# Kernel optimization log

Hardware: AMD Instinct MI355X
Metric: run time of the kernel (lower is better)

The kernel has to match this reference:

```python
import jax, jax.numpy as jnp
import numpy as np

N = 50000
E = 800000
F_IN = 128
HID = 128
NCLS = 40


def setup_inputs() -> dict:
    key = jax.random.key(0)
    ks = jax.random.split(key, 12)
    def glorot(k, fan_in, fan_out):
        s = jnp.sqrt(6.0 / (fan_in + fan_out))
        return jax.random.uniform(k, (fan_in, fan_out), jnp.float32, -s, s)
    x = jax.random.normal(ks[0], (N, F_IN), jnp.float32)
    edge_index = jax.random.randint(ks[1], (2, E), 0, N, jnp.int64)
    W1 = glorot(ks[2], F_IN, HID); b1 = jnp.zeros((HID,), jnp.float32)
    W2 = glorot(ks[3], HID, HID);  b2 = jnp.zeros((HID,), jnp.float32)
    W3 = glorot(ks[4], HID, HID);  b3 = jnp.zeros((HID,), jnp.float32)
    Wc = glorot(ks[5], HID, NCLS)
    bc = jnp.zeros((NCLS,), jnp.float32)
    return {"x": x, "edge_index": edge_index, "W1": W1, "b1": b1,
            "W2": W2, "b2": b2, "W3": W3, "b3": b3, "Wc": Wc, "bc": bc}


def _gcn_conv(h, src, dst, norm, W, b):
    # GCNConv: linear transform, then normalized scatter-add aggregation
    h = h @ W                              # [N, out]
    msg = h[src] * norm[:, None]           # [E+N, out] gathered + scaled
    out = jax.ops.segment_sum(msg, dst, num_segments=N)
    return out + b


def reference(x, edge_index, W1, b1, W2, b2, W3, b3, Wc, bc):
    # add self-loops (PyG GCNConv default) and compute symmetric norm once
    loop = jnp.arange(N, dtype=edge_index.dtype)
    src = jnp.concatenate([edge_index[0], loop])
    dst = jnp.concatenate([edge_index[1], loop])
    deg = jax.ops.segment_sum(jnp.ones_like(dst, dtype=x.dtype), dst, num_segments=N)
    dinv = jax.lax.rsqrt(deg)              # deg >= 1 due to self-loops
    norm = dinv[src] * dinv[dst]           # [E+N]

    h = jax.nn.relu(_gcn_conv(x, src, dst, norm, W1, b1))
    h = jax.nn.relu(_gcn_conv(h, src, dst, norm, W2, b2))
    h = jax.nn.relu(_gcn_conv(h, src, dst, norm, W3, b3))
    out = h @ Wc + bc
    return (out, h)
```

## Files before the change

### kernel.cpp

```cpp
#include <hip/hip_runtime.h>
#include <hip/hip_fp16.h>


#define FEAT 128

typedef _Float16 half_t;
typedef _Float16 f16x8 __attribute__((ext_vector_type(8)));
typedef float f32x16 __attribute__((ext_vector_type(16)));


__global__ __launch_bounds__(256) void k_count_rank(const int* __restrict__ dst,
                                                    int* __restrict__ deg,
                                                    int* __restrict__ rank, int E) {
  int e = blockIdx.x * 256 + threadIdx.x;
  if (e < E) rank[e] = atomicAdd(&deg[dst[e]], 1);
}

__global__ __launch_bounds__(256) void k_scanA(const int* __restrict__ deg,
                                               int* __restrict__ partial, int N) {
  __shared__ int s[256];
  int t = threadIdx.x;
  int i = blockIdx.x * 256 + t;
  s[t] = (i < N) ? deg[i] : 0;
  __syncthreads();
  for (int off = 128; off > 0; off >>= 1) {
    if (t < off) s[t] += s[t + off];
    __syncthreads();
  }
  if (t == 0) partial[blockIdx.x] = s[0];
}

__global__ __launch_bounds__(256) void k_scanB(int* __restrict__ partial, int nblk,
                                               int* __restrict__ offsets, int N) {
  __shared__ int s[256];
  int t = threadIdx.x;
  int v = (t < nblk) ? partial[t] : 0;
  s[t] = v;
  __syncthreads();
  for (int off = 1; off < 256; off <<= 1) {
    int x = (t >= off) ? s[t - off] : 0;
    __syncthreads();
    s[t] += x;
    __syncthreads();
  }
  if (t < nblk) partial[t] = s[t] - v;
  if (t == 0) offsets[N] = s[255];
}

__global__ __launch_bounds__(256) void k_scanC(const int* __restrict__ deg,
                                               const int* __restrict__ partial,
                                               int* __restrict__ offsets,
                                               float* __restrict__ dinv, int N) {
  __shared__ int s[256];
  int t = threadIdx.x;
  int i = blockIdx.x * 256 + t;
  int v = (i < N) ? deg[i] : 0;
  s[t] = v;
  __syncthreads();
  for (int off = 1; off < 256; off <<= 1) {
    int x = (t >= off) ? s[t - off] : 0;
    __syncthreads();
    s[t] += x;
    __syncthreads();
  }
  if (i < N) {
    offsets[i] = partial[blockIdx.x] + s[t] - v;
    dinv[i] = rsqrtf((float)(v + 1));
  }
}

__global__ __launch_bounds__(256) void k_place(const int* __restrict__ src,
                                               const int* __restrict__ dst,
                                               const int* __restrict__ offsets,
                                               const int* __restrict__ rank,
                                               int* __restrict__ col, int E) {
  int e = blockIdx.x * 256 + threadIdx.x;
  if (e < E) col[offsets[dst[e]] + rank[e]] = src[e];
}


__global__ __launch_bounds__(256) void k_prepW(const float* __restrict__ W1,
                                               const float* __restrict__ W2,
                                               const float* __restrict__ W3,
                                               half_t* __restrict__ Wt1,
                                               half_t* __restrict__ Wt2,
                                               half_t* __restrict__ Wt3) {
  int idx = blockIdx.x * 256 + threadIdx.x;
  int which = idx >> 14;
  int i = idx & 16383;
  int k = i >> 7, n = i & 127;
  const float* W = (which == 0) ? W1 : (which == 1) ? W2 : W3;
  half_t* Wt = (which == 0) ? Wt1 : (which == 1) ? Wt2 : Wt3;
  Wt[n * 128 + k] = (half_t)W[i];
}

template <int SRC_FP32>
__global__ __launch_bounds__(128) void k_gemm_mfma(const void* __restrict__ Asrc,
                                                   const half_t* __restrict__ Wt,
                                                   const float* __restrict__ dinv,
                                                   half_t* __restrict__ T,
                                                   int nrows) {
  __shared__ char lds[65536];
  char* sA = lds;
  char* sW = lds + 32768;
  int t = threadIdx.x;
  int rowBase = blockIdx.x * 128;
  int rowsHere = min(128, nrows - rowBase);

  #pragma unroll
  for (int i = 0; i < 16; ++i) {
    int lin = t + i * 128;
    int r = lin >> 4, c = lin & 15;
    *(float4*)(sW + r * 256 + ((c * 16) ^ ((r & 15) << 4))) =
        *(const float4*)((const char*)Wt + r * 256 + c * 16);
  }
  if (SRC_FP32) {
    const float* Af = (const float*)Asrc;
    #pragma unroll
    for (int i = 0; i < 16; ++i) {
      int lin = t + i * 128;
      int r = lin >> 4, c = lin & 15;
      f16x8 h = {};
      if (r < rowsHere) {
        const float4* p = (const float4*)(Af + (size_t)(rowBase + r) * FEAT + c * 8);
        float4 v0 = p[0], v1 = p[1];
        h[0] = (half_t)v0.x; h[1] = (half_t)v0.y; h[2] = (half_t)v0.z; h[3] = (half_t)v0.w;
        h[4] = (half_t)v1.x; h[5] = (half_t)v1.y; h[6] = (half_t)v1.z; h[7] = (half_t)v1.w;
      }
      *(f16x8*)(sA + r * 256 + ((c * 16) ^ ((r & 15) << 4))) = h;
    }
  } else {
    const char* Ah = (const char*)Asrc;
    #pragma unroll
    for (int i = 0; i < 16; ++i) {
      int lin = t + i * 128;
      int r = lin >> 4, c = lin & 15;
      float4 v = {};
      if (r < rowsHere) v = *(const float4*)(Ah + (size_t)(rowBase + r) * 256 + c * 16);
      *(float4*)(sA + r * 256 + ((c * 16) ^ ((r & 15) << 4))) = v;
    }
  }
  __syncthreads();

  int wv = t >> 6;
  int l = t & 63;
  int l31 = l & 31;
  int lhi = l >> 5;
  int sw = (l31 & 15) << 4;

  f32x16 acc[2][4] = {};

  #pragma unroll
  for (int step = 0; step < 8; ++step) {
    int koff = step * 32 + lhi * 16;
    int ko = koff ^ sw;
    f16x8 a0 = *(const f16x8*)(sA + (wv * 64 + l31) * 256 + ko);
    f16x8 a1 = *(const f16x8*)(sA + (wv * 64 + 32 + l31) * 256 + ko);
    f16x8 b0 = *(const f16x8*)(sW + (l31) * 256 + ko);
    f16x8 b1 = *(const f16x8*)(sW + (32 + l31) * 256 + ko);
    f16x8 b2 = *(const f16x8*)(sW + (64 + l31) * 256 + ko);
    f16x8 b3 = *(const f16x8*)(sW + (96 + l31) * 256 + ko);
    acc[0][0] = __builtin_amdgcn_mfma_f32_32x32x16_f16(a0, b0, acc[0][0], 0, 0, 0);
    acc[0][1] = __builtin_amdgcn_mfma_f32_32x32x16_f16(a0, b1, acc[0][1], 0, 0, 0);
    acc[0][2] = __builtin_amdgcn_mfma_f32_32x32x16_f16(a0, b2, acc[0][2], 0, 0, 0);
    acc[0][3] = __builtin_amdgcn_mfma_f32_32x32x16_f16(a0, b3, acc[0][3], 0, 0, 0);
    acc[1][0] = __builtin_amdgcn_mfma_f32_32x32x16_f16(a1, b0, acc[1][0], 0, 0, 0);
    acc[1][1] = __builtin_amdgcn_mfma_f32_32x32x16_f16(a1, b1, acc[1][1], 0, 0, 0);
    acc[1][2] = __builtin_amdgcn_mfma_f32_32x32x16_f16(a1, b2, acc[1][2], 0, 0, 0);
    acc[1][3] = __builtin_amdgcn_mfma_f32_32x32x16_f16(a1, b3, acc[1][3], 0, 0, 0);
  }

  #pragma unroll
  for (int m = 0; m < 2; ++m) {
    #pragma unroll
    for (int j = 0; j < 16; ++j) {
      int rloc = wv * 64 + m * 32 + (j & 3) + 8 * (j >> 2) + 4 * lhi;
      if (rloc < rowsHere) {
        int grow = rowBase + rloc;
        float d = dinv[grow];
        #pragma unroll
        for (int n = 0; n < 4; ++n) {
          T[(size_t)grow * FEAT + n * 32 + l31] = (half_t)(acc[m][n][j] * d);
        }
      }
    }
  }
}

template <int OUTF>
__global__ __launch_bounds__(256) void k_aggregate(const __half2* __restrict__ T2,
                                                   const int* __restrict__ offsets,
                                                   const int* __restrict__ col,
                                                   const float* __restrict__ dinv,
                                                   const float* __restrict__ bias,
                                                   float* __restrict__ outF,
                                                   __half2* __restrict__ outH,
                                                   int N) {
  int wave = threadIdx.x >> 6;
  int lane = threadIdx.x & 63;
  int node = blockIdx.x * 4 + wave;
  if (node >= N) return;
  int e0 = offsets[node], e1 = offsets[node + 1];

  __half2 sv = T2[(size_t)node * 64 + lane];
  float ax = __half2float(sv.x), ay = __half2float(sv.y);

  int e = e0;
  for (; e + 8 <= e1; e += 8) {
    int s0 = col[e + 0], s1 = col[e + 1], s2 = col[e + 2], s3 = col[e + 3];
    int s4 = col[e + 4], s5 = col[e + 5], s6 = col[e + 6], s7 = col[e + 7];
    __half2 v0 = T2[(size_t)s0 * 64 + lane];
    __half2 v1 = T2[(size_t)s1 * 64 + lane];
    __half2 v2 = T2[(size_t)s2 * 64 + lane];
    __half2 v3 = T2[(size_t)s3 * 64 + lane];
    __half2 v4 = T2[(size_t)s4 * 64 + lane];
    __half2 v5 = T2[(size_t)s5 * 64 + lane];
    __half2 v6 = T2[(size_t)s6 * 64 + lane];
    __half2 v7 = T2[(size_t)s7 * 64 + lane];
    float x01 = __half2float(v0.x) + __half2float(v1.x);
    float x23 = __half2float(v2.x) + __half2float(v3.x);
    float x45 = __half2float(v4.x) + __half2float(v5.x);
    float x67 = __half2float(v6.x) + __half2float(v7.x);
    float y01 = __half2float(v0.y) + __half2float(v1.y);
    float y23 = __half2float(v2.y) + __half2float(v3.y);
    float y45 = __half2float(v4.y) + __half2float(v5.y);
    float y67 = __half2float(v6.y) + __half2float(v7.y);
    ax += (x01 + x23) + (x45 + x67);
    ay += (y01 + y23) + (y45 + y67);
  }
  for (; e + 2 <= e1; e += 2) {
    __half2 v0 = T2[(size_t)col[e] * 64 + lane];
    __half2 v1 = T2[(size_t)col[e + 1] * 64 + lane];
    ax += __half2float(v0.x) + __half2float(v1.x);
    ay += __half2float(v0.y) + __half2float(v1.y);
  }
  if (e < e1) {
    __half2 v = T2[(size_t)col[e] * 64 + lane];
    ax += __half2float(v.x);
    ay += __half2float(v.y);
  }

  float di = dinv[node];
  float2 b = ((const float2*)bias)[lane];
  float ox = fmaxf(di * ax + b.x, 0.f);
  float oy = fmaxf(di * ay + b.y, 0.f);
  if (OUTF) {
    *(float2*)&outF[(size_t)node * FEAT + 2 * lane] = make_float2(ox, oy);
  } else {
    outH[(size_t)node * 64 + lane] = __floats2half2_rn(ox, oy);
  }
}

__global__ __launch_bounds__(256) void k_classifier(const float* __restrict__ h,
                                                    const float* __restrict__ Wc,
                                                    const float* __restrict__ bc,
                                                    float* __restrict__ out, int N) {
  __shared__ float sh[64 * 132];
  __shared__ float sWt[40 * 130];
  int t = threadIdx.x;
  int nodeBase = blockIdx.x * 64;
  int nodesHere = min(64, N - nodeBase);

  for (int i = t; i < FEAT * 40; i += 256) {
    int k = i / 40, c = i - k * 40;
    sWt[c * 130 + k] = Wc[i];
  }
  {
    const float4* H4 = (const float4*)(h + (size_t)nodeBase * FEAT);
    #pragma unroll
    for (int i = 0; i < 8; ++i) {
      int lin = t + i * 256;
      int r = lin >> 5, kc = lin & 31;
      float4 v = make_float4(0.f, 0.f, 0.f, 0.f);
      if (r < nodesHere) v = H4[lin];
      *(float4*)&sh[r * 132 + kc * 4] = v;
    }
  }
  __syncthreads();

  int n0 = (t >> 3) * 2;
  int cg = (t & 7) * 5;
  float acc0[5], acc1[5];
  #pragma unroll
  for (int j = 0; j < 5; ++j) { acc0[j] = bc[cg + j]; acc1[j] = acc0[j]; }

  #pragma unroll 4
  for (int k4 = 0; k4 < 32; ++k4) {
    float4 h0 = *(const float4*)&sh[n0 * 132 + k4 * 4];
    float4 h1 = *(const float4*)&sh[(n0 + 1) * 132 + k4 * 4];
    #pragma unroll
    for (int j = 0; j < 5; ++j) {
      float4 w = *(const float4*)&sWt[(cg + j) * 130 + k4 * 4];
      acc0[j] += h0.x * w.x + h0.y * w.y + h0.z * w.z + h0.w * w.w;
      acc1[j] += h1.x * w.x + h1.y * w.y + h1.z * w.z + h1.w * w.w;
    }
  }

  if (n0 < nodesHere) {
    float* o = out + (size_t)(nodeBase + n0) * 40 + cg;
    #pragma unroll
    for (int j = 0; j < 5; ++j) o[j] = acc0[j];
  }
  if (n0 + 1 < nodesHere) {
    float* o = out + (size_t)(nodeBase + n0 + 1) * 40 + cg;
    #pragma unroll
    for (int j = 0; j < 5; ++j) o[j] = acc1[j];
  }
}


extern "C" void kernel_launch(void* const* d_in, const int* in_sizes, int n_in,
                              void* d_out, int out_size, void* d_ws, size_t ws_size,
                              hipStream_t stream) {
  const float* x    = (const float*)d_in[0];
  const int*   edge = (const int*)d_in[1];
  const float* W1   = (const float*)d_in[2];
  const float* b1   = (const float*)d_in[3];
  const float* W2   = (const float*)d_in[4];
  const float* b2   = (const float*)d_in[5];
  const float* W3   = (const float*)d_in[6];
  const float* b3   = (const float*)d_in[7];
  const float* Wc   = (const float*)d_in[8];
  const float* bc   = (const float*)d_in[9];

  int N = in_sizes[0] / FEAT;
  int E = in_sizes[1] / 2;

  float* out  = (float*)d_out;
  float* hOut = out + (size_t)N * 40;

  size_t o = 0;
  char* wsb = (char*)d_ws;
  auto take = [&](size_t bytes) -> void* {
    void* p = wsb + o;
    o += (bytes + 255) & ~(size_t)255;
    return p;
  };
  float*   dinv    = (float*)take((size_t)N * 4);
  int*     deg     = (int*)take((size_t)N * 4);
  int*     rank    = (int*)take((size_t)E * 4);
  int*     partial = (int*)take(256 * 4);
  int*     offsets = (int*)take(((size_t)N + 8) * 4);
  int*     col     = (int*)take((size_t)E * 4);
  half_t*  T2h     = (half_t*)take((size_t)N * FEAT * 2);
  half_t*  Bh      = (half_t*)take((size_t)N * FEAT * 2);
  half_t*  Wt1     = (half_t*)take(16384 * 2);
  half_t*  Wt2     = (half_t*)take(16384 * 2);
  half_t*  Wt3     = (half_t*)take(16384 * 2);

  const int* e_src = edge;
  const int* e_dst = edge + E;

  hipMemsetAsync(deg, 0, (size_t)N * 4, stream);

  int nblk = (N + 255) / 256;
  int eblk = (E + 255) / 256;

  k_prepW<<<192, 256, 0, stream>>>(W1, W2, W3, Wt1, Wt2, Wt3);
  k_count_rank<<<eblk, 256, 0, stream>>>(e_dst, deg, rank, E);
  k_scanA<<<nblk, 256, 0, stream>>>(deg, partial, N);
  k_scanB<<<1, 256, 0, stream>>>(partial, nblk, offsets, N);
  k_scanC<<<nblk, 256, 0, stream>>>(deg, partial, offsets, dinv, N);
  k_place<<<eblk, 256, 0, stream>>>(e_src, e_dst, offsets, rank, col, E);

  int gblk = (N + 127) / 128;
  int ablk = (N + 3) / 4;
  __half2* T2 = (__half2*)T2h;
  k_gemm_mfma<1><<<gblk, 128, 0, stream>>>(x, Wt1, dinv, T2h, N);
  k_aggregate<0><<<ablk, 256, 0, stream>>>(T2, offsets, col, dinv, b1, nullptr,
                                           (__half2*)Bh, N);
  k_gemm_mfma<0><<<gblk, 128, 0, stream>>>(Bh, Wt2, dinv, T2h, N);
  k_aggregate<0><<<ablk, 256, 0, stream>>>(T2, offsets, col, dinv, b2, nullptr,
                                           (__half2*)Bh, N);
  k_gemm_mfma<0><<<gblk, 128, 0, stream>>>(Bh, Wt3, dinv, T2h, N);
  k_aggregate<1><<<ablk, 256, 0, stream>>>(T2, offsets, col, dinv, b3, hOut,
                                           nullptr, N);
  k_classifier<<<(N + 63) / 64, 256, 0, stream>>>(hOut, Wc, bc, out, N);
}
```

Before: 245.6 us.

## Process two nodes per wave in aggregation, widen GEMM blocks, fuse deg memset

The aggregation kernel now assigns half a wave (32 lanes) per node and has each lane load 8 bytes (4 halves) per neighbour row. This halves the number of waves and raises the bytes moved per gather instruction. The GEMM kernel now uses 256 threads per 128-row tile, with each wave computing 32 rows instead of 64. That lowers accumulator register pressure and doubles the waves per tile. The deg memset is folded into the weight-prep kernel to remove one launch, though the two half-wave nodes in a wave can now diverge when their degrees differ.

Measured after the change: 230.3 us. 6.2% less time.

```diff
diff --git a/kernel.cpp b/kernel.cpp
--- a/kernel.cpp
+++ b/kernel.cpp
@@ -7,6 +7,26 @@
 typedef _Float16 half_t;
 typedef _Float16 f16x8 __attribute__((ext_vector_type(8)));
 typedef float f32x16 __attribute__((ext_vector_type(16)));
+
+
+__global__ __launch_bounds__(256) void k_prep(const float* __restrict__ W1,
+                                              const float* __restrict__ W2,
+                                              const float* __restrict__ W3,
+                                              half_t* __restrict__ Wt1,
+                                              half_t* __restrict__ Wt2,
+                                              half_t* __restrict__ Wt3,
+                                              int* __restrict__ deg, int N) {
+  int idx = blockIdx.x * 256 + threadIdx.x;
+  if (idx < N) deg[idx] = 0;
+  if (idx < 3 * 16384) {
+    int which = idx >> 14;
+    int i = idx & 16383;
+    int k = i >> 7, n = i & 127;
+    const float* W = (which == 0) ? W1 : (which == 1) ? W2 : W3;
+    half_t* Wt = (which == 0) ? Wt1 : (which == 1) ? Wt2 : Wt3;
+    Wt[n * 128 + k] = (half_t)W[i];
+  }
+}
 
 
 __global__ __launch_bounds__(256) void k_count_rank(const int* __restrict__ dst,
@@ -78,24 +98,8 @@
   if (e < E) col[offsets[dst[e]] + rank[e]] = src[e];
 }
 
-
-__global__ __launch_bounds__(256) void k_prepW(const float* __restrict__ W1,
-                                               const float* __restrict__ W2,
-                                               const float* __restrict__ W3,
-                                               half_t* __restrict__ Wt1,
-                                               half_t* __restrict__ Wt2,
-                                               half_t* __restrict__ Wt3) {
-  int idx = blockIdx.x * 256 + threadIdx.x;
-  int which = idx >> 14;
-  int i = idx & 16383;
-  int k = i >> 7, n = i & 127;
-  const float* W = (which == 0) ? W1 : (which == 1) ? W2 : W3;
-  half_t* Wt = (which == 0) ? Wt1 : (which == 1) ? Wt2 : Wt3;
-  Wt[n * 128 + k] = (half_t)W[i];
-}
-
 template <int SRC_FP32>
-__global__ __launch_bounds__(128) void k_gemm_mfma(const void* __restrict__ Asrc,
+__global__ __launch_bounds__(256) void k_gemm_mfma(const void* __restrict__ Asrc,
                                                    const half_t* __restrict__ Wt,
                                                    const float* __restrict__ dinv,
                                                    half_t* __restrict__ T,
@@ -108,8 +112,8 @@
   int rowsHere = min(128, nrows - rowBase);
 
   #pragma unroll
-  for (int i = 0; i < 16; ++i) {
-    int lin = t + i * 128;
+  for (int i = 0; i < 8; ++i) {
+    int lin = t + i * 256;
     int r = lin >> 4, c = lin & 15;
     *(float4*)(sW + r * 256 + ((c * 16) ^ ((r & 15) << 4))) =
         *(const float4*)((const char*)Wt + r * 256 + c * 16);
@@ -117,8 +121,8 @@
   if (SRC_FP32) {
     const float* Af = (const float*)Asrc;
     #pragma unroll
-    for (int i = 0; i < 16; ++i) {
-      int lin = t + i * 128;
+    for (int i = 0; i < 8; ++i) {
+      int lin = t + i * 256;
       int r = lin >> 4, c = lin & 15;
       f16x8 h = {};
       if (r < rowsHere) {
@@ -132,8 +136,8 @@
   } else {
     const char* Ah = (const char*)Asrc;
     #pragma unroll
-    for (int i = 0; i < 16; ++i) {
-      int lin = t + i * 128;
+    for (int i = 0; i < 8; ++i) {
+      int lin = t + i * 256;
       int r = lin >> 4, c = lin & 15;
       float4 v = {};
       if (r < rowsHere) v = *(const float4*)(Ah + (size_t)(rowBase + r) * 256 + c * 16);
@@ -148,106 +152,98 @@
   int lhi = l >> 5;
   int sw = (l31 & 15) << 4;
 
-  f32x16 acc[2][4] = {};
+  f32x16 acc[4] = {};
 
   #pragma unroll
   for (int step = 0; step < 8; ++step) {
-    int koff = step * 32 + lhi * 16;
-    int ko = koff ^ sw;
-    f16x8 a0 = *(const f16x8*)(sA + (wv * 64 + l31) * 256 + ko);
-    f16x8 a1 = *(const f16x8*)(sA + (wv * 64 + 32 + l31) * 256 + ko);
+    int ko = (step * 32 + lhi * 16) ^ sw;
+    f16x8 a  = *(const f16x8*)(sA + (wv * 32 + l31) * 256 + ko);
     f16x8 b0 = *(const f16x8*)(sW + (l31) * 256 + ko);
     f16x8 b1 = *(const f16x8*)(sW + (32 + l31) * 256 + ko);
     f16x8 b2 = *(const f16x8*)(sW + (64 + l31) * 256 + ko);
     f16x8 b3 = *(const f16x8*)(sW + (96 + l31) * 256 + ko);
-    acc[0][0] = __builtin_amdgcn_mfma_f32_32x32x16_f16(a0, b0, acc[0][0], 0, 0, 0);
-    acc[0][1] = __builtin_amdgcn_mfma_f32_32x32x16_f16(a0, b1, acc[0][1], 0, 0, 0);
-    acc[0][2] = __builtin_amdgcn_mfma_f32_32x32x16_f16(a0, b2, acc[0][2], 0, 0, 0);
-    acc[0][3] = __builtin_amdgcn_mfma_f32_32x32x16_f16(a0, b3, acc[0][3], 0, 0, 0);
-    acc[1][0] = __builtin_amdgcn_mfma_f32_32x32x16_f16(a1, b0, acc[1][0], 0, 0, 0);
-    acc[1][1] = __builtin_amdgcn_mfma_f32_32x32x16_f16(a1, b1, acc[1][1], 0, 0, 0);
-    acc[1][2] = __builtin_amdgcn_mfma_f32_32x32x16_f16(a1, b2, acc[1][2], 0, 0, 0);
-    acc[1][3] = __builtin_amdgcn_mfma_f32_32x32x16_f16(a1, b3, acc[1][3], 0, 0, 0);
+    acc[0] = __builtin_amdgcn_mfma_f32_32x32x16_f16(a, b0, acc[0], 0, 0, 0);
+    acc[1] = __builtin_amdgcn_mfma_f32_32x32x16_f16(a, b1, acc[1], 0, 0, 0);
+    acc[2] = __builtin_amdgcn_mfma_f32_32x32x16_f16(a, b2, acc[2], 0, 0, 0);
+    acc[3] = __builtin_amdgcn_mfma_f32_32x32x16_f16(a, b3, acc[3], 0, 0, 0);
   }
 
   #pragma unroll
-  for (int m = 0; m < 2; ++m) {
-    #pragma unroll
-    for (int j = 0; j < 16; ++j) {
-      int rloc = wv * 64 + m * 32 + (j & 3) + 8 * (j >> 2) + 4 * lhi;
-      if (rloc < rowsHere) {
-        int grow = rowBase + rloc;
-        float d = dinv[grow];
-        #pragma unroll
-        for (int n = 0; n < 4; ++n) {
-          T[(size_t)grow * FEAT + n * 32 + l31] = (half_t)(acc[m][n][j] * d);
-        }
+  for (int j = 0; j < 16; ++j) {
+    int rloc = wv * 32 + (j & 3) + 8 * (j >> 2) + 4 * lhi;
+    if (rloc < rowsHere) {
+      int grow = rowBase + rloc;
+      float d = dinv[grow];
+      #pragma unroll
+      for (int n = 0; n < 4; ++n) {
+        T[(size_t)grow * FEAT + n * 32 + l31] = (half_t)(acc[n][j] * d);
       }
     }
   }
 }
 
 template <int OUTF>
-__global__ __launch_bounds__(256) void k_aggregate(const __half2* __restrict__ T2,
+__global__ __launch_bounds__(256) void k_aggregate(const uint2* __restrict__ T4,
                                                    const int* __restrict__ offsets,
                                                    const int* __restrict__ col,
                                                    const float* __restrict__ dinv,
                                                    const float* __restrict__ bias,
-                                                   float* __restrict__ outF,
-                                                   __half2* __restrict__ outH,
+                                                   float4* __restrict__ outF,
+                                                   uint2* __restrict__ outH,
                                                    int N) {
   int wave = threadIdx.x >> 6;
-  int lane = threadIdx.x & 63;
-  int node = blockIdx.x * 4 + wave;
+  int half = (threadIdx.x >> 5) & 1;
+  int q = threadIdx.x & 31;
+  int node = (blockIdx.x * 4 + wave) * 2 + half;
   if (node >= N) return;
   int e0 = offsets[node], e1 = offsets[node + 1];
 
-  __half2 sv = T2[(size_t)node * 64 + lane];
-  float ax = __half2float(sv.x), ay = __half2float(sv.y);
+  uint2 sv = T4[(size_t)node * 32 + q];
+  __half2 h0 = *(__half2*)&sv.x, h1 = *(__half2*)&sv.y;
+  float ax = __half2float(h0.x), ay = __half2float(h0.y);
+  float az = __half2float(h1.x), aw = __half2float(h1.y);
 
   int e = e0;
   for (; e + 8 <= e1; e += 8) {
     int s0 = col[e + 0], s1 = col[e + 1], s2 = col[e + 2], s3 = col[e + 3];
     int s4 = col[e + 4], s5 = col[e + 5], s6 = col[e + 6], s7 = col[e + 7];
-    __half2 v0 = T2[(size_t)s0 * 64 + lane];
-    __half2 v1 = T2[(size_t)s1 * 64 + lane];
-    __half2 v2 = T2[(size_t)s2 * 64 + lane];
-    __half2 v3 = T2[(size_t)s3 * 64 + lane];
-    __half2 v4 = T2[(size_t)s4 * 64 + lane];
-    __half2 v5 = T2[(size_t)s5 * 64 + lane];
-    __half2 v6 = T2[(size_t)s6 * 64 + lane];
-    __half2 v7 = T2[(size_t)s7 * 64 + lane];
-    float x01 = __half2float(v0.x) + __half2float(v1.x);
-    float x23 = __half2float(v2.x) + __half2float(v3.x);
-    float x45 = __half2float(v4.x) + __half2float(v5.x);
-    float x67 = __half2float(v6.x) + __half2float(v7.x);
-    float y01 = __half2float(v0.y) + __half2float(v1.y);
-    float y23 = __half2float(v2.y) + __half2float(v3.y);
-    float y45 = __half2float(v4.y) + __half2float(v5.y);
-    float y67 = __half2float(v6.y) + __half2float(v7.y);
-    ax += (x01 + x23) + (x45 + x67);
-    ay += (y01 + y23) + (y45 + y67);
-  }
-  for (; e + 2 <= e1; e += 2) {
-    __half2 v0 = T2[(size_t)col[e] * 64 + lane];
-    __half2 v1 = T2[(size_t)col[e + 1] * 64 + lane];
-    ax += __half2float(v0.x) + __half2float(v1.x);
-    ay += __half2float(v0.y) + __half2float(v1.y);
-  }
-  if (e < e1) {
-    __half2 v = T2[(size_t)col[e] * 64 + lane];
-    ax += __half2float(v.x);
-    ay += __half2float(v.y);
+    uint2 v0 = T4[(size_t)s0 * 32 + q];
+    uint2 v1 = T4[(size_t)s1 * 32 + q];
+    uint2 v2 = T4[(size_t)s2 * 32 + q];
+    uint2 v3 = T4[(size_t)s3 * 32 + q];
+    uint2 v4 = T4[(size_t)s4 * 32 + q];
+    uint2 v5 = T4[(size_t)s5 * 32 + q];
+    uint2 v6 = T4[(size_t)s6 * 32 + q];
+    uint2 v7 = T4[(size_t)s7 * 32 + q];
+    #pragma unroll
+    for (int u = 0; u < 8; ++u) {
+      uint2 v = (u == 0) ? v0 : (u == 1) ? v1 : (u == 2) ? v2 : (u == 3) ? v3
+              : (u == 4) ? v4 : (u == 5) ? v5 : (u == 6) ? v6 : v7;
+      __half2 p0 = *(__half2*)&v.x, p1 = *(__half2*)&v.y;
+      ax += __half2float(p0.x); ay += __half2float(p0.y);
+      az += __half2float(p1.x); aw += __half2float(p1.y);
+    }
+  }
+  for (; e < e1; ++e) {
+    uint2 v = T4[(size_t)col[e] * 32 + q];
+    __half2 p0 = *(__half2*)&v.x, p1 = *(__half2*)&v.y;
+    ax += __half2float(p0.x); ay += __half2float(p0.y);
+    az += __half2float(p1.x); aw += __half2float(p1.y);
   }
 
   float di = dinv[node];
-  float2 b = ((const float2*)bias)[lane];
+  float4 b = ((const float4*)bias)[q];
   float ox = fmaxf(di * ax + b.x, 0.f);
   float oy = fmaxf(di * ay + b.y, 0.f);
+  float oz = fmaxf(di * az + b.z, 0.f);
+  float ow = fmaxf(di * aw + b.w, 0.f);
   if (OUTF) {
-    *(float2*)&outF[(size_t)node * FEAT + 2 * lane] = make_float2(ox, oy);
+    outF[(size_t)node * 32 + q] = make_float4(ox, oy, oz, ow);
   } else {
-    outH[(size_t)node * 64 + lane] = __floats2half2_rn(ox, oy);
+    uint2 o;
+    __half2 t0 = __floats2half2_rn(ox, oy), t1 = __floats2half2_rn(oz, ow);
+    o.x = *(unsigned*)&t0; o.y = *(unsigned*)&t1;
+    outH[(size_t)node * 32 + q] = o;
   }
 }
 
@@ -351,12 +347,10 @@
   const int* e_src = edge;
   const int* e_dst = edge + E;
 
-  hipMemsetAsync(deg, 0, (size_t)N * 4, stream);
-
   int nblk = (N + 255) / 256;
   int eblk = (E + 255) / 256;
 
-  k_prepW<<<192, 256, 0, stream>>>(W1, W2, W3, Wt1, Wt2, Wt3);
+  k_prep<<<nblk, 256, 0, stream>>>(W1, W2, W3, Wt1, Wt2, Wt3, deg, N);
   k_count_rank<<<eblk, 256, 0, stream>>>(e_dst, deg, rank, E);
   k_scanA<<<nblk, 256, 0, stream>>>(deg, partial, N);
   k_scanB<<<1, 256, 0, stream>>>(partial, nblk, offsets, N);
@@ -364,16 +358,16 @@
   k_place<<<eblk, 256, 0, stream>>>(e_src, e_dst, offsets, rank, col, E);
 
   int gblk = (N + 127) / 128;
-  int ablk = (N + 3) / 4;
-  __half2* T2 = (__half2*)T2h;
-  k_gemm_mfma<1><<<gblk, 128, 0, stream>>>(x, Wt1, dinv, T2h, N);
-  k_aggregate<0><<<ablk, 256, 0, stream>>>(T2, offsets, col, dinv, b1, nullptr,
-                                           (__half2*)Bh, N);
-  k_gemm_mfma<0><<<gblk, 128, 0, stream>>>(Bh, Wt2, dinv, T2h, N);
-  k_aggregate<0><<<ablk, 256, 0, stream>>>(T2, offsets, col, dinv, b2, nullptr,
-                                           (__half2*)Bh, N);
-  k_gemm_mfma<0><<<gblk, 128, 0, stream>>>(Bh, Wt3, dinv, T2h, N);
-  k_aggregate<1><<<ablk, 256, 0, stream>>>(T2, offsets, col, dinv, b3, hOut,
-                                           nullptr, N);
+  int ablk = (N + 7) / 8;
+  uint2* T4 = (uint2*)T2h;
+  k_gemm_mfma<1><<<gblk, 256, 0, stream>>>(x, Wt1, dinv, T2h, N);
+  k_aggregate<0><<<ablk, 256, 0, stream>>>(T4, offsets, col, dinv, b1, nullptr,
+                                           (uint2*)Bh, N);
+  k_gemm_mfma<0><<<gblk, 256, 0, stream>>>(Bh, Wt2, dinv, T2h, N);
+  k_aggregate<0><<<ablk, 256, 0, stream>>>(T4, offsets, col, dinv, b2, nullptr,
+                                           (uint2*)Bh, N);
+  k_gemm_mfma<0><<<gblk, 256, 0, stream>>>(Bh, Wt3, dinv, T2h, N);
+  k_aggregate<1><<<ablk, 256, 0, stream>>>(T4, offsets, col, dinv, b3,
+                                           (float4*)hOut, nullptr, N);
   k_classifier<<<(N + 63) / 64, 256, 0, stream>>>(hOut, Wc, bc, out, N);
 }
```
